# Performance work log

Measured on AMD Instinct MI355X. Metric: run time of the kernel, lower is better.

## Reference

```python
import math
import jax, jax.numpy as jnp
import numpy as np

B, S, D, H, L = 2, 2048, 1024, 16, 4
HD = D // H  # head_dim = 64


def setup_inputs() -> dict:
    key = jax.random.key(0)
    ks = jax.random.split(key, 7)
    scale = 0.02
    return {
        "x": jax.random.normal(ks[0], (B, S, D), jnp.float32),
        "past_q": jax.random.normal(ks[1], (B, H, S, L, HD), jnp.float32),
        "past_v": jax.random.normal(ks[2], (B, H, S, L, HD), jnp.float32),
        "Wq": jax.random.normal(ks[3], (D, D), jnp.float32) * scale,
        "bq": jnp.zeros((D,), jnp.float32),
        "Wo": jax.random.normal(ks[4], (D, D), jnp.float32) * scale,
        "bo": jnp.zeros((D,), jnp.float32),
    }


def reference(x, past_q, past_v, Wq, bq, Wo, bo):
    b, s, d = x.shape
    # q_proj then split heads -> [B,H,S,hd]
    q = (x @ Wq.T + bq).reshape(b, s, H, HD).transpose(0, 2, 1, 3)
    v = x.reshape(b, s, H, HD).transpose(0, 2, 1, 3)
    inv = 1.0 / math.sqrt(HD)
    # token scores: Q used as both query and key, causal mask
    token_scores = jnp.einsum("bhqd,bhkd->bhqk", q, q) * inv
    causal = jnp.triu(jnp.ones((s, s), bool), k=1)
    token_scores = jnp.where(causal, -jnp.inf, token_scores)
    # memory scores: elementwise mul-sum over L cached layers -> [B,H,S,L]
    mem_scores = jnp.einsum("bhsd,bhsld->bhsl", q, past_q) * inv
    scores = jnp.concatenate([token_scores, mem_scores], axis=-1)  # [B,H,S,S+L]
    weights = jax.nn.softmax(scores, axis=-1)
    tw, mw = weights[..., :s], weights[..., s:]
    token_ctx = jnp.einsum("bhqk,bhkd->bhqd", tw, v)
    mem_ctx = jnp.einsum("bhsl,bhsld->bhsd", mw, past_v)
    ctx = (token_ctx + mem_ctx).transpose(0, 2, 1, 3).reshape(b, s, d)
    return jax.nn.gelu(ctx @ Wo.T + bo, approximate=False)
```

## Files before the change

kernel.cpp:

```cpp
#include <hip/hip_runtime.h>
#include <hip/hip_bf16.h>
#include <math.h>

#define S_LEN 2048
#define DIM   1024
#define NH    16
#define NL    4
#define NB    2
#define PARTS_PER_BH 80
#define ALPHA 0.42466086f

typedef __attribute__((ext_vector_type(8))) short bf16x8;
typedef __attribute__((ext_vector_type(4))) float f32x4;
typedef unsigned short u16;

template <int N> struct Tag { static constexpr int cur = N; };

__device__ __forceinline__ float bf2f(u16 u) {
  union { unsigned int i; float f; } x; x.i = ((unsigned int)u) << 16; return x.f;
}
__device__ __forceinline__ u16 f2bf(float f) {
  union { float f; unsigned int i; } x; x.f = f;
  unsigned int r = x.i + 0x7fffu + ((x.i >> 16) & 1u);
  return (u16)(r >> 16);
}
__device__ __forceinline__ u16 f2bfq(float f) {
  __hip_bfloat16 h = __float2bfloat16(f);
  return *reinterpret_cast<u16*>(&h);
}

__device__ __forceinline__ void g2l16(const void* g, void* l) {
  __builtin_amdgcn_global_load_lds(
      (const __attribute__((address_space(1))) void*)g,
      (__attribute__((address_space(3))) void*)l, 16, 0, 0);
}

__device__ __forceinline__ float gelu_fast(float v) {
  float y = 0.79788456f * (v + 0.044715f * v * v * v);
  float e = exp2f(y * 2.88539008f);
  float t = 1.0f - 2.0f / (e + 1.0f);
  return 0.5f * v * (1.0f + t);
}

__global__ __launch_bounds__(256)
void cvt_all(const float* __restrict__ x, const float* __restrict__ wq,
             const float* __restrict__ wo, u16* __restrict__ ox,
             u16* __restrict__ owq, u16* __restrict__ owo, int n4x, int n4w) {
  int i = blockIdx.x * blockDim.x + threadIdx.x;
  const float* src; u16* dst; int j;
  if (i < n4x)            { src = x;  dst = ox;  j = i; }
  else if (i < n4x + n4w) { src = wq; dst = owq; j = i - n4x; }
  else                    { src = wo; dst = owo; j = i - n4x - n4w;
                            if (j >= n4w) return; }
  float4 v = ((const float4*)src)[j];
  ushort4 o;
  o.x = f2bf(v.x); o.y = f2bf(v.y); o.z = f2bf(v.z); o.w = f2bf(v.w);
  ((ushort4*)dst)[j] = o;
}

template <bool GELU, typename OT>
__global__ __launch_bounds__(256)
void gemm_bt(const u16* __restrict__ A, const u16* __restrict__ Bt,
             const float* __restrict__ bias, OT* __restrict__ C,
             int M, int N, int K, float oscale) {
  __shared__ u16 As[2][128 * 64];
  __shared__ u16 Bs[2][64 * 64];
  const int lane = threadIdx.x & 63, wave = threadIdx.x >> 6;
  const int ln = lane & 15, g = lane >> 4;
  const int m0 = blockIdx.y * 128, n0 = blockIdx.x * 64;
  const int wm = wave >> 1, wn = wave & 1;
  f32x4 acc[4][2] = {};

  auto stage = [&](int buf, int k0) {
#pragma unroll
    for (int rd = 0; rd < 6; ++rd) {
      int ch = rd * 4 + wave;
      if (ch < 16) {
        int flatb = ch * 1024 + lane * 16;
        int row = flatb >> 7;
        int within = (flatb & 127) ^ ((row & 7) << 4);
        g2l16((const char*)A + ((size_t)(m0 + row) * K + k0) * 2 + within,
              (char*)As[buf] + ch * 1024);
      } else {
        int flatb = (ch - 16) * 1024 + lane * 16;
        int row = flatb >> 7;
        int within = (flatb & 127) ^ ((row & 7) << 4);
        g2l16((const char*)Bt + ((size_t)(n0 + row) * K + k0) * 2 + within,
              (char*)Bs[buf] + (ch - 16) * 1024);
      }
    }
  };

  stage(0, 0);
  __syncthreads();
  const int NT = K / 64;
  for (int t = 0; t < NT; ++t) {
    const int cur = t & 1;
    if (t + 1 < NT) stage(cur ^ 1, (t + 1) * 64);
#pragma unroll
    for (int kc = 0; kc < 2; ++kc) {
      bf16x8 af[4], bfr[2];
#pragma unroll
      for (int i = 0; i < 4; ++i) {
        int ra = wm * 64 + i * 16 + ln;
        af[i] = *(const bf16x8*)((const char*)As[cur] + ra * 128 +
                                 ((kc * 64 + g * 16) ^ ((ra & 7) << 4)));
      }
#pragma unroll
      for (int j = 0; j < 2; ++j) {
        int rb = wn * 32 + j * 16 + ln;
        bfr[j] = *(const bf16x8*)((const char*)Bs[cur] + rb * 128 +
                                  ((kc * 64 + g * 16) ^ ((rb & 7) << 4)));
      }
#pragma unroll
      for (int i = 0; i < 4; ++i)
#pragma unroll
        for (int j = 0; j < 2; ++j)
          acc[i][j] = __builtin_amdgcn_mfma_f32_16x16x32_bf16(af[i], bfr[j], acc[i][j], 0, 0, 0);
    }
    __syncthreads();
  }

#pragma unroll
  for (int j = 0; j < 2; ++j) {
    int gc = n0 + wn * 32 + j * 16 + ln;
    float bv = bias[gc];
#pragma unroll
    for (int i = 0; i < 4; ++i) {
      int gr0 = m0 + wm * 64 + i * 16 + g * 4;
#pragma unroll
      for (int r = 0; r < 4; ++r) {
        float v = acc[i][j][r] + bv;
        if constexpr (GELU) v = gelu_fast(v);
        v *= oscale;
        if constexpr (sizeof(OT) == 2) C[(size_t)(gr0 + r) * N + gc] = (OT)f2bf(v);
        else                           C[(size_t)(gr0 + r) * N + gc] = (OT)v;
      }
    }
  }
}

__global__ __launch_bounds__(256, 4)
void attn(const u16* __restrict__ Q, const u16* __restrict__ Xb,
          u16* __restrict__ CTXP, float* __restrict__ MP, float* __restrict__ LP) {
  __shared__ __attribute__((aligned(16))) char lds[40960];

  const int lane = threadIdx.x & 63, wave = threadIdx.x >> 6;
  const int ln = lane & 15, g = lane >> 4;
  const int h = blockIdx.y, b = blockIdx.z;

  const int p = blockIdx.x;
  int qt, chunk;
  if (p < 8)       { qt = p;                          chunk = 0; }
  else if (p < 24) { int i = p - 8;  qt = 8 + (i >> 1);  chunk = i & 1; }
  else if (p < 48) { int i = p - 24; qt = 16 + i / 3;    chunk = i % 3; }
  else             { int i = p - 48; qt = 24 + (i >> 2); chunk = i & 3; }
  const int kt0 = chunk * 8;
  const int kt1e = kt0 + 8 < qt + 1 ? kt0 + 8 : qt + 1;

  const size_t qrow = (size_t)b * S_LEN + qt * 64 + wave * 16 + ln;
  const bf16x8 qa0 = *(const bf16x8*)(Q + qrow * DIM + h * 64 + g * 8);
  const bf16x8 qa1 = *(const bf16x8*)(Q + qrow * DIM + h * 64 + 32 + g * 8);

  const int tid = threadIdx.x;
  const int vr0 = (tid >> 3) * 2;
  const int vc0 = (tid & 7) * 8;
  const int t7 = tid & 7;
  const int sw7 = (ln & 7) << 4;
  const int kbase0 = ln * 128 + ((g * 16) ^ sw7);
  const int kbase1 = ln * 128 + ((64 + g * 16) ^ sw7);
  const int swb = (ln & 7) ^ (ln >> 3);
  int vrd0[4], vrd1[4];
#pragma unroll
  for (int ns = 0; ns < 4; ++ns) {
    int sw = (swb ^ (ns * 2)) << 4;
    vrd0[ns] = ln * 128 + ((g * 16) ^ sw);
    vrd1[ns] = ln * 128 + ((64 + g * 16) ^ sw);
  }
  int vwr[8];
#pragma unroll
  for (int j = 0; j < 8; ++j)
    vwr[j] = (vc0 + j) * 128 + ((vr0 * 2) ^ ((j ^ t7) << 4));
  int pst[4];
#pragma unroll
  for (int sub = 0; sub < 4; ++sub)
    pst[sub] = 32768 + wave * 2048 + ln * 128 + ((sub * 32 + g * 8) ^ sw7);
  const int prd0 = 32768 + wave * 2048 + ln * 128 + ((g * 16) ^ sw7);
  const int prd1 = 32768 + wave * 2048 + ln * 128 + ((64 + g * 16) ^ sw7);
  int ksrc[2];
#pragma unroll
  for (int rd = 0; rd < 2; ++rd) {
    int ch = rd * 4 + wave;
    int flat = ch * 1024 + lane * 16;
    int row = flat >> 7;
    ksrc[rd] = row * (DIM * 2) + ((flat & 127) ^ ((row & 7) << 4));
  }

  const size_t STEP = (size_t)64 * DIM * 2;
  const char* kq = (const char*)(Q + ((size_t)b * S_LEN + (size_t)kt0 * 64) * DIM + h * 64);
  const char* xv = (const char*)(Xb + ((size_t)b * S_LEN + (size_t)kt0 * 64 + vr0) * DIM + h * 64 + vc0);

  f32x4 acc[4] = {};
  float m_run = -INFINITY;
  float l_run = 0.f;

  {
    bf16x8 r0 = *(const bf16x8*)xv;
    bf16x8 r1 = *(const bf16x8*)(xv + DIM * 2);
#pragma unroll
    for (int rd = 0; rd < 2; ++rd)
      g2l16(kq + ksrc[rd], lds + (rd * 4 + wave) * 1024);
#pragma unroll
    for (int j = 0; j < 8; ++j) {
      unsigned int pack = (unsigned int)(u16)r0[j] | ((unsigned int)(u16)r1[j] << 16);
      *(unsigned int*)(lds + 16384 + vwr[j]) = pack;
    }
  }
  __syncthreads();

  int kt = kt0;
  auto body = [&](auto tag) {
    constexpr int CUR = decltype(tag)::cur;
    constexpr int NXT = CUR ^ 1;
    const bool more = (kt + 1 < kt1e);
    bf16x8 nr0, nr1;
    if (more) {
      const char* nxv = xv + STEP;
      nr0 = *(const bf16x8*)nxv;
      nr1 = *(const bf16x8*)(nxv + DIM * 2);
      const char* nkq = kq + STEP;
#pragma unroll
      for (int rd = 0; rd < 2; ++rd)
        g2l16(nkq + ksrc[rd], lds + NXT * 8192 + (rd * 4 + wave) * 1024);
      __builtin_amdgcn_sched_barrier(0);
    }

    float pv_[4][4];
    __builtin_amdgcn_s_setprio(1);
#pragma unroll
    for (int sub = 0; sub < 4; ++sub) {
      bf16x8 kb0 = *(const bf16x8*)(lds + CUR * 8192 + sub * 2048 + kbase0);
      bf16x8 kb1 = *(const bf16x8*)(lds + CUR * 8192 + sub * 2048 + kbase1);
      f32x4 c = {};
      c = __builtin_amdgcn_mfma_f32_16x16x32_bf16(kb0, qa0, c, 0, 0, 0);
      c = __builtin_amdgcn_mfma_f32_16x16x32_bf16(kb1, qa1, c, 0, 0, 0);
      if (kt == qt) {
#pragma unroll
        for (int r = 0; r < 4; ++r) {
          int key = sub * 16 + g * 4 + r;
          pv_[sub][r] = (key > wave * 16 + ln) ? -INFINITY : c[r];
        }
      } else {
#pragma unroll
        for (int r = 0; r < 4; ++r) pv_[sub][r] = c[r];
      }
    }
    __builtin_amdgcn_s_setprio(0);

    float pmax = pv_[0][0];
#pragma unroll
    for (int sub = 0; sub < 4; ++sub)
#pragma unroll
      for (int r = 0; r < 4; ++r) pmax = fmaxf(pmax, pv_[sub][r]);
    pmax = fmaxf(pmax, __shfl_xor(pmax, 16));
    pmax = fmaxf(pmax, __shfl_xor(pmax, 32));

    if (!__all(pmax <= m_run + 8.0f)) {
      float m_new = fmaxf(m_run, pmax);
      float scl = exp2f(m_run - m_new);
      m_run = m_new;
      l_run *= scl;
#pragma unroll
      for (int r = 0; r < 4; ++r) {
        float s = __shfl(scl, g * 4 + r);
#pragma unroll
        for (int ns = 0; ns < 4; ++ns) acc[ns][r] *= s;
      }
    }

    float lsum = 0.f;
#pragma unroll
    for (int sub = 0; sub < 4; ++sub)
#pragma unroll
      for (int r = 0; r < 4; ++r) {
        pv_[sub][r] = exp2f(pv_[sub][r] - m_run);
        lsum += pv_[sub][r];
      }
    lsum += __shfl_xor(lsum, 16);
    lsum += __shfl_xor(lsum, 32);
    l_run += lsum;

#pragma unroll
    for (int sub = 0; sub < 4; ++sub) {
      uint2 val;
      val.x = (unsigned int)f2bfq(pv_[sub][0]) | ((unsigned int)f2bfq(pv_[sub][1]) << 16);
      val.y = (unsigned int)f2bfq(pv_[sub][2]) | ((unsigned int)f2bfq(pv_[sub][3]) << 16);
      *(uint2*)(lds + pst[sub]) = val;
    }

    bf16x8 pa0 = *(const bf16x8*)(lds + prd0);
    bf16x8 pa1 = *(const bf16x8*)(lds + prd1);
    __builtin_amdgcn_s_setprio(1);
#pragma unroll
    for (int ns = 0; ns < 4; ++ns) {
      bf16x8 vb0 = *(const bf16x8*)(lds + 16384 + CUR * 8192 + ns * 2048 + vrd0[ns]);
      bf16x8 vb1 = *(const bf16x8*)(lds + 16384 + CUR * 8192 + ns * 2048 + vrd1[ns]);
      acc[ns] = __builtin_amdgcn_mfma_f32_16x16x32_bf16(pa0, vb0, acc[ns], 0, 0, 0);
      acc[ns] = __builtin_amdgcn_mfma_f32_16x16x32_bf16(pa1, vb1, acc[ns], 0, 0, 0);
    }
    __builtin_amdgcn_s_setprio(0);

    if (more) {
#pragma unroll
      for (int j = 0; j < 8; ++j) {
        unsigned int pack = (unsigned int)(u16)nr0[j] | ((unsigned int)(u16)nr1[j] << 16);
        *(unsigned int*)(lds + 16384 + NXT * 8192 + vwr[j]) = pack;
      }
    }
    __syncthreads();
    kq += STEP; xv += STEP;
  };

  for (;;) {
    body(Tag<0>{});
    if (++kt >= kt1e) break;
    body(Tag<1>{});
    if (++kt >= kt1e) break;
  }

  const size_t slot = ((size_t)(b * NH + h)) * PARTS_PER_BH + p;
#pragma unroll
  for (int ns = 0; ns < 4; ++ns)
#pragma unroll
    for (int r = 0; r < 4; ++r) {
      int qr = wave * 16 + g * 4 + r;
      CTXP[slot * 4096 + (size_t)qr * 64 + ns * 16 + ln] = f2bfq(acc[ns][r]);
    }
  if (lane < 16) {
    MP[slot * 64 + wave * 16 + lane] = m_run;
    LP[slot * 64 + wave * 16 + lane] = l_run;
  }
}

__global__ __launch_bounds__(256)
void finalize(const u16* __restrict__ Q, const float* __restrict__ PQ,
              const float* __restrict__ PV, const u16* __restrict__ CTXP,
              const float* __restrict__ MP, const float* __restrict__ LP,
              u16* __restrict__ Cout) {
  const int lane = threadIdx.x & 63, wave = threadIdx.x >> 6;
  const size_t row = (size_t)blockIdx.x * 4 + wave;
  const int s = (int)(row & (S_LEN - 1));
  const int h = (int)((row >> 11) & (NH - 1));
  const int b = (int)(row >> 15);

  const int qt = s >> 6, G = qt >> 3, parts = G + 1;
  const int baseG[4] = {0, 8, 24, 48};
  const int p0 = baseG[G] + (qt & 7) * parts;
  const size_t slot0 = ((size_t)(b * NH + h)) * PARTS_PER_BH + p0;
  const int sr = s & 63;

  float mc[4], lc[4];
  float m_tok = -INFINITY;
#pragma unroll
  for (int c = 0; c < 4; ++c)
    if (c < parts) {
      mc[c] = MP[(slot0 + c) * 64 + sr];
      lc[c] = LP[(slot0 + c) * 64 + sr];
      m_tok = fmaxf(m_tok, mc[c]);
    }
  float l_tok = 0.f, cd = 0.f;
#pragma unroll
  for (int c = 0; c < 4; ++c)
    if (c < parts) {
      float w = exp2f(mc[c] - m_tok);
      l_tok += w * lc[c];
      cd += w * bf2f(CTXP[(slot0 + c) * 4096 + (size_t)sr * 64 + lane]);
    }

  const float qd = bf2f(Q[((size_t)b * S_LEN + s) * DIM + h * 64 + lane]);
  const float* pq = PQ + row * (NL * 64);
  const float* pv = PV + row * (NL * 64);
  float msc[NL];
  float m_fin = m_tok;
#pragma unroll
  for (int lm = 0; lm < NL; ++lm) {
    float prod = qd * pq[lm * 64 + lane];
#pragma unroll
    for (int o = 1; o < 64; o <<= 1) prod += __shfl_xor(prod, o);
    msc[lm] = prod * ALPHA;
    m_fin = fmaxf(m_fin, msc[lm]);
  }
  const float a = exp2f(m_tok - m_fin);
  float l_fin = l_tok * a;
  cd *= a;
#pragma unroll
  for (int lm = 0; lm < NL; ++lm) {
    float w = exp2f(msc[lm] - m_fin);
    l_fin += w;
    cd += w * pv[lm * 64 + lane];
  }
  Cout[((size_t)b * S_LEN + s) * DIM + h * 64 + lane] = f2bf(cd / l_fin);
}

extern "C" void kernel_launch(void* const* d_in, const int* in_sizes, int n_in,
                              void* d_out, int out_size, void* d_ws, size_t ws_size,
                              hipStream_t stream) {
  const float* x  = (const float*)d_in[0];
  const float* pq = (const float*)d_in[1];
  const float* pv = (const float*)d_in[2];
  const float* Wq = (const float*)d_in[3];
  const float* bq = (const float*)d_in[4];
  const float* Wo = (const float*)d_in[5];
  const float* bo = (const float*)d_in[6];
  float* out = (float*)d_out;

  const int M = NB * S_LEN;
  u16*   Qws  = (u16*)d_ws;
  u16*   Cws  = Qws + (size_t)M * DIM;
  u16*   xbf  = Cws + (size_t)M * DIM;
  u16*   Wqbf = xbf + (size_t)M * DIM;
  u16*   Wobf = Wqbf + (size_t)DIM * DIM;
  u16*   CTXP = Wobf + (size_t)DIM * DIM;
  float* MP   = (float*)(CTXP + (size_t)NB * NH * PARTS_PER_BH * 4096);
  float* LP   = MP + (size_t)NB * NH * PARTS_PER_BH * 64;

  const int n4x = M * DIM / 4, n4w = DIM * DIM / 4;
  cvt_all<<<(n4x + 2 * n4w + 255) / 256, 256, 0, stream>>>(
      x, Wq, Wo, xbf, Wqbf, Wobf, n4x, n4w);

  gemm_bt<false, u16><<<dim3(DIM / 64, M / 128), 256, 0, stream>>>(
      xbf, Wqbf, bq, Qws, M, DIM, DIM, ALPHA);
  attn<<<dim3(PARTS_PER_BH, NH, NB), 256, 0, stream>>>(Qws, xbf, CTXP, MP, LP);
  finalize<<<NB * NH * S_LEN / 4, 256, 0, stream>>>(Qws, pq, pv, CTXP, MP, LP, Cws);
  gemm_bt<true, float><<<dim3(DIM / 64, M / 128), 256, 0, stream>>>(
      Cws, Wobf, bo, out, M, DIM, DIM, 1.0f);
}
```

Baseline: 129.7 us.

## Reverse attn block order, balance chunk split, use DPP row reductions in finalize

The attention kernel now issues its partitions in reverse order, so the heaviest query tiles start first, and it splits each query tile's key range evenly across its parts instead of using fixed 8-tile chunks. In finalize, the four memory-score dot products are computed at once. Each 16-lane group handles one cached layer using vectorized loads and a DPP row reduction, which replaces four 64-lane shuffle reductions. The goal is to cut tail imbalance in attn and shuffle overhead in finalize.

```diff
diff --git a/kernel.cpp b/kernel.cpp
--- a/kernel.cpp
+++ b/kernel.cpp
@@ -33,6 +33,21 @@
   __builtin_amdgcn_global_load_lds(
       (const __attribute__((address_space(1))) void*)g,
       (__attribute__((address_space(3))) void*)l, 16, 0, 0);
+}
+
+template <int CTRL>
+__device__ __forceinline__ float dppf(float x) {
+  union { float f; int i; } u, r;
+  u.f = x;
+  r.i = __builtin_amdgcn_update_dpp(0, u.i, CTRL, 0xF, 0xF, true);
+  return r.f;
+}
+__device__ __forceinline__ float rsum16(float x) {
+  x += dppf<0xB1>(x);
+  x += dppf<0x4E>(x);
+  x += dppf<0x141>(x);
+  x += dppf<0x140>(x);
+  return x;
 }
 
 __device__ __forceinline__ float gelu_fast(float v) {
@@ -149,14 +164,16 @@
   const int ln = lane & 15, g = lane >> 4;
   const int h = blockIdx.y, b = blockIdx.z;
 
-  const int p = blockIdx.x;
+  const int pl = PARTS_PER_BH - 1 - blockIdx.x;
   int qt, chunk;
-  if (p < 8)       { qt = p;                          chunk = 0; }
-  else if (p < 24) { int i = p - 8;  qt = 8 + (i >> 1);  chunk = i & 1; }
-  else if (p < 48) { int i = p - 24; qt = 16 + i / 3;    chunk = i % 3; }
-  else             { int i = p - 48; qt = 24 + (i >> 2); chunk = i & 3; }
-  const int kt0 = chunk * 8;
-  const int kt1e = kt0 + 8 < qt + 1 ? kt0 + 8 : qt + 1;
+  if (pl < 8)       { qt = pl;                           chunk = 0; }
+  else if (pl < 24) { int i = pl - 8;  qt = 8 + (i >> 1);  chunk = i & 1; }
+  else if (pl < 48) { int i = pl - 24; qt = 16 + i / 3;    chunk = i % 3; }
+  else              { int i = pl - 48; qt = 24 + (i >> 2); chunk = i & 3; }
+  const int len = qt + 1;
+  const int parts = (len + 7) >> 3;
+  const int kt0 = (chunk * len) / parts;
+  const int kt1e = ((chunk + 1) * len) / parts;
 
   const size_t qrow = (size_t)b * S_LEN + qt * 64 + wave * 16 + ln;
   const bf16x8 qa0 = *(const bf16x8*)(Q + qrow * DIM + h * 64 + g * 8);
@@ -328,7 +345,7 @@
     if (++kt >= kt1e) break;
   }
 
-  const size_t slot = ((size_t)(b * NH + h)) * PARTS_PER_BH + p;
+  const size_t slot = ((size_t)(b * NH + h)) * PARTS_PER_BH + pl;
 #pragma unroll
   for (int ns = 0; ns < 4; ++ns)
 #pragma unroll
@@ -348,6 +365,7 @@
               const float* __restrict__ MP, const float* __restrict__ LP,
               u16* __restrict__ Cout) {
   const int lane = threadIdx.x & 63, wave = threadIdx.x >> 6;
+  const int ln = lane & 15, g = lane >> 4;
   const size_t row = (size_t)blockIdx.x * 4 + wave;
   const int s = (int)(row & (S_LEN - 1));
   const int h = (int)((row >> 11) & (NH - 1));
@@ -359,6 +377,14 @@
   const size_t slot0 = ((size_t)(b * NH + h)) * PARTS_PER_BH + p0;
   const int sr = s & 63;
 
+  const float* pq = PQ + row * (NL * 64);
+  const float* pv = PV + row * (NL * 64);
+  ushort4 qu = *(const ushort4*)(Q + ((size_t)b * S_LEN + s) * DIM + h * 64 + ln * 4);
+  float4 pqv = *(const float4*)(pq + g * 64 + ln * 4);
+  float prod = bf2f(qu.x) * pqv.x + bf2f(qu.y) * pqv.y +
+               bf2f(qu.z) * pqv.z + bf2f(qu.w) * pqv.w;
+  prod = rsum16(prod);
+
   float mc[4], lc[4];
   float m_tok = -INFINITY;
 #pragma unroll
@@ -377,17 +403,11 @@
       cd += w * bf2f(CTXP[(slot0 + c) * 4096 + (size_t)sr * 64 + lane]);
     }
 
-  const float qd = bf2f(Q[((size_t)b * S_LEN + s) * DIM + h * 64 + lane]);
-  const float* pq = PQ + row * (NL * 64);
-  const float* pv = PV + row * (NL * 64);
   float msc[NL];
   float m_fin = m_tok;
 #pragma unroll
   for (int lm = 0; lm < NL; ++lm) {
-    float prod = qd * pq[lm * 64 + lane];
-#pragma unroll
-    for (int o = 1; o < 64; o <<= 1) prod += __shfl_xor(prod, o);
-    msc[lm] = prod * ALPHA;
+    msc[lm] = __shfl(prod, lm << 4) * ALPHA;
     m_fin = fmaxf(m_fin, msc[lm]);
   }
   const float a = exp2f(m_tok - m_fin);
```

New measurement: 127.6 us. About the same (-1.7%).
